# Kernel optimization log

Hardware: AMD Instinct MI355X
Metric: run time of the kernel (lower is better)

## Reference

```python
import jax, jax.numpy as jnp
import numpy as np

N_NODES = 50000
N_PAIRS = 800000
D = 64          # node feature dim
N_BASIS = 8     # basis functions per pair


def setup_inputs() -> dict:
    key = jax.random.key(0)
    k1, k2, k3, k4, k5, k6 = jax.random.split(key, 6)
    p1 = jax.random.normal(k1, (N_NODES, D), dtype=jnp.float32)
    pair_i = jax.random.randint(k2, (N_PAIRS,), 0, N_NODES, dtype=jnp.int64)
    pair_j = jax.random.randint(k3, (N_PAIRS,), 0, N_NODES, dtype=jnp.int64)
    basis = jax.random.normal(k4, (N_PAIRS, N_BASIS), dtype=jnp.float32)
    # bias-free MLP: 64 -> 256 -> 512 (= D * N_BASIS), scaled init
    W1 = jax.random.normal(k5, (D, 256), dtype=jnp.float32) / np.sqrt(D)
    W2 = jax.random.normal(k6, (256, D * N_BASIS), dtype=jnp.float32) / np.sqrt(256.0)
    return {"p1": p1, "pair_i": pair_i, "pair_j": pair_j, "basis": basis,
            "W1": W1, "W2": W2}


def reference(p1, pair_i, pair_j, basis, W1, W2):
    # gather node features for both ends of each pair and sum -> [n_pairs, D]
    inter = p1[pair_i] + p1[pair_j]
    # bias-free FeedForward with tanh between layers
    h = jnp.tanh(inter @ W1)          # [n_pairs, 256]
    h = h @ W2                        # [n_pairs, D * N_BASIS]
    h = h.reshape(-1, p1.shape[-1], basis.shape[-1])  # [n_pairs, D, n_basis]
    out = jnp.einsum('icb,ib->ic', h, basis)          # [n_pairs, D]
    return out[:, None, :]            # [n_pairs, 1, D]
```

## Files before the change

kernel.cpp:

```cpp
#include <hip/hip_runtime.h>

typedef unsigned short u16;
typedef unsigned int   u32;
typedef __bf16 bf16x8 __attribute__((ext_vector_type(8)));
typedef float  f32x4  __attribute__((ext_vector_type(4)));
typedef float  f32x2  __attribute__((ext_vector_type(2)));
typedef unsigned short u16x8 __attribute__((ext_vector_type(8)));
typedef unsigned int   u32x2 __attribute__((ext_vector_type(2)));

#define PPB 128
#define CPB 5

__device__ __forceinline__ u16 f2bf(float f){
  union { float f; u32 i; } v; v.f = f;
  u32 u = v.i;
  u += 0x7fffu + ((u >> 16) & 1u);
  return (u16)(u >> 16);
}
__device__ __forceinline__ float tanh_fast(float x){
  x = fminf(fmaxf(x, -12.f), 12.f);
  float t = __builtin_amdgcn_exp2f(x * 2.885390081777926815f);
  return (t - 1.f) * __builtin_amdgcn_rcpf(t + 1.f);
}

__global__ __launch_bounds__(256) void transpose_cast_k(
    const float* __restrict__ in, u16* __restrict__ out, int R, int C)
{
  __shared__ u16 tile[64][65];
  const int tx = threadIdx.x & 63;
  const int ty = threadIdx.x >> 6;
  const int c0 = blockIdx.x * 64;
  const int r0 = blockIdx.y * 64;
#pragma unroll
  for (int rr = 0; rr < 16; ++rr){
    int r = ty + rr * 4;
    tile[r][tx] = f2bf(in[(size_t)(r0 + r) * C + c0 + tx]);
  }
  __syncthreads();
#pragma unroll
  for (int rr = 0; rr < 16; ++rr){
    int r = ty + rr * 4;
    out[(size_t)(c0 + r) * R + r0 + tx] = tile[tx][r];
  }
}

__global__ __launch_bounds__(256) void w2_block_k(
    const float* __restrict__ in, u16* __restrict__ out)
{
  __shared__ float tile[32][65];
  const int kk = blockIdx.x;
  const int n0 = blockIdx.y * 64;
  const int t  = threadIdx.x;
  {
    int r  = t >> 3;
    int c8 = t & 7;
    const float* src = in + (size_t)(kk*32 + r)*512 + n0 + c8*8;
    f32x4 v0 = *(const f32x4*)src;
    f32x4 v1 = *(const f32x4*)(src + 4);
#pragma unroll
    for (int e = 0; e < 4; ++e){
      tile[r][c8*8 + e]     = v0[e];
      tile[r][c8*8 + 4 + e] = v1[e];
    }
  }
  __syncthreads();
  {
    int c = t >> 2, part = t & 3;
    u16x8 o;
#pragma unroll
    for (int e = 0; e < 8; ++e) o[e] = f2bf(tile[part*8 + e][c]);
    *(u16x8*)(out + ((size_t)kk*512 + n0 + c)*32 + part*8) = o;
  }
}

__global__ __launch_bounds__(1024, 4) void pilayer_kernel(
    const float* __restrict__ p1,
    const int* __restrict__ pair_i,
    const int* __restrict__ pair_j,
    const float* __restrict__ basis,
    const u16* __restrict__ w1t,
    const u16* __restrict__ w2b,
    float* __restrict__ out,
    int n_pairs)
{
  extern __shared__ __align__(16) u16 smem[];
  u16* sh_h  = smem;
  u16* sh_i0 = smem + PPB * 256;
  u16* sh_i1 = sh_i0 + PPB * 64;

  const int tid  = threadIdx.x;
  const int blk  = blockIdx.x;
  const int lane = tid & 63;
  const int w    = tid >> 6;
  const int m16  = lane & 15;
  const int q    = lane >> 4;
  const int sw3  = m16 & 7;
  const int cw   = (w*2 + (q >> 1)) ^ m16;

  bf16x8 awf[8][2];
#pragma unroll
  for (int kk = 0; kk < 8; ++kk)
#pragma unroll
    for (int nt = 0; nt < 2; ++nt)
      awf[kk][nt] = *(const bf16x8*)(
          w2b + ((size_t)kk*512 + w*32 + nt*16 + m16)*32 + q*8);
  const u16* arow = w1t + (size_t)(w*16 + m16)*64 + q*8;
  bf16x8 af0 = *(const bf16x8*)(arow);
  bf16x8 af1 = *(const bf16x8*)(arow + 32);
  __builtin_amdgcn_sched_barrier(0);

  const int pbase = blk * CPB * PPB;
  const int m_g   = tid >> 3;
  const int seg_g = tid & 7;

  {
    int p = pbase + m_g;
    if (p >= n_pairs) p = n_pairs - 1;
    const float* si = p1 + (size_t)pair_i[p]*64 + seg_g*8;
    const float* sj = p1 + (size_t)pair_j[p]*64 + seg_g*8;
    f32x4 a0 = ((const f32x4*)si)[0], a1 = ((const f32x4*)si)[1];
    f32x4 b0 = ((const f32x4*)sj)[0], b1 = ((const f32x4*)sj)[1];
    u16x8 r;
#pragma unroll
    for (int e = 0; e < 4; ++e){
      r[e]     = f2bf(a0[e] + b0[e]);
      r[e + 4] = f2bf(a1[e] + b1[e]);
    }
    *(u16x8*)(sh_i0 + m_g*64 + ((seg_g ^ (m_g & 7)) * 8)) = r;
  }
  __syncthreads();

  u16* sin_cur = sh_i0;
  u16* sin_nxt = sh_i1;
  int nxt_i = 0, nxt_j = 0;

  for (int t = 0; t < CPB; ++t){
    const int pb = pbase + t * PPB;
    const bool pf = (t + 1 < CPB);

    if (pf){
      int pn = pb + PPB + m_g;
      if (pn >= n_pairs) pn = n_pairs - 1;
      nxt_i = pair_i[pn];
      nxt_j = pair_j[pn];
      asm volatile("" : "+v"(nxt_i), "+v"(nxt_j));
    }
    for (int mt1 = 0; mt1 < PPB/16; ++mt1){
      const u16* irow = sin_cur + (size_t)(mt1*16 + m16) * 64;
      bf16x8 b0 = *(const bf16x8*)(irow + ((q ^ sw3) * 8));
      bf16x8 b1 = *(const bf16x8*)(irow + (((q + 4) ^ sw3) * 8));
      f32x4 acc = {0.f, 0.f, 0.f, 0.f};
      acc = __builtin_amdgcn_mfma_f32_16x16x32_bf16(af0, b0, acc, 0, 0, 0);
      acc = __builtin_amdgcn_mfma_f32_16x16x32_bf16(af1, b1, acc, 0, 0, 0);
      u32 lo = (u32)f2bf(tanh_fast(acc[0])) | ((u32)f2bf(tanh_fast(acc[1])) << 16);
      u32 hi = (u32)f2bf(tanh_fast(acc[2])) | ((u32)f2bf(tanh_fast(acc[3])) << 16);
      u32x2 pk = {lo, hi};
      *(u32x2*)(sh_h + (size_t)(mt1*16 + m16)*256 + cw*8 + (q & 1)*4) = pk;
    }
    __syncthreads();

    f32x4 gi0, gi1, gj0, gj1;
    if (pf){
      const float* si = p1 + (size_t)(u32)nxt_i*64 + seg_g*8;
      const float* sj = p1 + (size_t)(u32)nxt_j*64 + seg_g*8;
      gi0 = ((const f32x4*)si)[0]; gi1 = ((const f32x4*)si)[1];
      gj0 = ((const f32x4*)sj)[0]; gj1 = ((const f32x4*)sj)[1];
      asm volatile("" : "+v"(gi0), "+v"(gi1), "+v"(gj0), "+v"(gj1));
    }

    for (int mt = 0; mt < PPB/16; ++mt){
      const int row = mt*16 + m16;
      const int mg  = pb + row;
      const int mgc = (mg < n_pairs) ? mg : (n_pairs - 1);
      f32x4 bb = *(const f32x4*)(basis + (size_t)mgc*8 + (q & 1)*4);

      const u16* hbase = sh_h + (size_t)row * 256;
      f32x4 acc0 = {0.f, 0.f, 0.f, 0.f};
      f32x4 acc1 = {0.f, 0.f, 0.f, 0.f};

      bf16x8 bh = *(const bf16x8*)(hbase + ((q ^ m16) * 8));
#pragma unroll
      for (int kk = 0; kk < 8; ++kk){
        bf16x8 bhn;
        if (kk < 7) bhn = *(const bf16x8*)(hbase + ((((kk + 1)*4 + q) ^ m16) * 8));
        acc0 = __builtin_amdgcn_mfma_f32_16x16x32_bf16(awf[kk][0], bh, acc0, 0, 0, 0);
        acc1 = __builtin_amdgcn_mfma_f32_16x16x32_bf16(awf[kk][1], bh, acc1, 0, 0, 0);
        bh = bhn;
      }

#pragma unroll
      for (int nt = 0; nt < 2; ++nt){
        f32x4 a = (nt == 0) ? acc0 : acc1;
        float s = a[0]*bb[0] + a[1]*bb[1] + a[2]*bb[2] + a[3]*bb[3];
        s += __shfl_xor(s, 16);
        float v2 = __shfl_xor(s, 32);
        if (q == 0 && mg < n_pairs){
          f32x2 pk = {s, v2};
          *(f32x2*)(out + (size_t)mg*64 + w*4 + nt*2) = pk;
        }
      }
    }

    if (pf){
      u16x8 r;
#pragma unroll
      for (int e = 0; e < 4; ++e){
        r[e]     = f2bf(gi0[e] + gj0[e]);
        r[e + 4] = f2bf(gi1[e] + gj1[e]);
      }
      *(u16x8*)(sin_nxt + m_g*64 + ((seg_g ^ (m_g & 7)) * 8)) = r;
    }
    __syncthreads();
    u16* tmp = sin_cur; sin_cur = sin_nxt; sin_nxt = tmp;
  }
}

extern "C" void kernel_launch(void* const* d_in, const int* in_sizes, int n_in,
                              void* d_out, int out_size, void* d_ws, size_t ws_size,
                              hipStream_t stream)
{
  const float* p1    = (const float*)d_in[0];
  const int*   pi    = (const int*)d_in[1];
  const int*   pj    = (const int*)d_in[2];
  const float* basis = (const float*)d_in[3];
  const float* W1    = (const float*)d_in[4];
  const float* W2    = (const float*)d_in[5];
  float* out = (float*)d_out;

  u16* w1t = (u16*)d_ws;
  u16* w2b = w1t + 64 * 256;

  const int n_pairs = in_sizes[1];
  const int lds_bytes = (PPB * 256 + 2 * PPB * 64) * (int)sizeof(u16);

  static int attr_done = 0;
  if (!attr_done){
    hipFuncSetAttribute((const void*)pilayer_kernel,
                        hipFuncAttributeMaxDynamicSharedMemorySize, lds_bytes);
    attr_done = 1;
  }

  transpose_cast_k<<<dim3(4, 1), 256, 0, stream>>>(W1, w1t, 64, 256);
  w2_block_k<<<dim3(8, 8), 256, 0, stream>>>(W2, w2b);

  const int n_chunks = (n_pairs + PPB - 1) / PPB;
  const int blocks   = (n_chunks + CPB - 1) / CPB;
  pilayer_kernel<<<blocks, 1024, lds_bytes, stream>>>(
      p1, pi, pj, basis, w1t, w2b, out, n_pairs);
}
```

Before: 680.0 us.

## Prefetch gathered node rows via direct global-to-LDS loads across chunk pipeline

Replaces the register-staged prefetch of next-chunk node features with global_load_lds async copies into a raw fp32 LDS buffer, issued before the first GEMM. The pair indices are loaded two chunks ahead. Also simplifies tanh (drops the clamp, uses 1-2/(t+1)), switches to hardware bf16 packing, and software-pipelines the basis loads. The goal is to hide gather latency and free VGPRs. The cost is 64KB more LDS per block, which may reduce occupancy, plus an extra barrier per chunk.

```diff
diff --git a/kernel.cpp b/kernel.cpp
--- a/kernel.cpp
+++ b/kernel.cpp
@@ -7,6 +7,7 @@
 typedef float  f32x2  __attribute__((ext_vector_type(2)));
 typedef unsigned short u16x8 __attribute__((ext_vector_type(8)));
 typedef unsigned int   u32x2 __attribute__((ext_vector_type(2)));
+typedef unsigned int   u32x4 __attribute__((ext_vector_type(4)));
 
 #define PPB 128
 #define CPB 5
@@ -17,10 +18,19 @@
   u += 0x7fffu + ((u >> 16) & 1u);
   return (u16)(u >> 16);
 }
+__device__ __forceinline__ u32 pkbf(float lo, float hi){
+  union { __bf16 h[2]; u32 u; } v;
+  v.h[0] = (__bf16)lo; v.h[1] = (__bf16)hi;
+  return v.u;
+}
 __device__ __forceinline__ float tanh_fast(float x){
-  x = fminf(fmaxf(x, -12.f), 12.f);
   float t = __builtin_amdgcn_exp2f(x * 2.885390081777926815f);
-  return (t - 1.f) * __builtin_amdgcn_rcpf(t + 1.f);
+  return __builtin_fmaf(-2.f, __builtin_amdgcn_rcpf(t + 1.f), 1.f);
+}
+__device__ __forceinline__ void gload16(const float* gp, u16* lp){
+  __builtin_amdgcn_global_load_lds(
+      (const __attribute__((address_space(1))) u32*)gp,
+      (__attribute__((address_space(3))) u32*)lp, 16, 0, 0);
 }
 
 __global__ __launch_bounds__(256) void transpose_cast_k(
@@ -84,9 +94,10 @@
     int n_pairs)
 {
   extern __shared__ __align__(16) u16 smem[];
-  u16* sh_h  = smem;
-  u16* sh_i0 = smem + PPB * 256;
-  u16* sh_i1 = sh_i0 + PPB * 64;
+  u16*   sh_h     = smem;
+  u16*   sh_inter = smem + PPB * 256;
+  float* raw      = (float*)(sh_inter + PPB*64);
+  u16*   raw_u16  = (u16*)raw;
 
   const int tid  = threadIdx.x;
   const int blk  = blockIdx.x;
@@ -97,6 +108,13 @@
   const int sw3  = m16 & 7;
   const int cw   = (w*2 + (q >> 1)) ^ m16;
 
+  const int reg_r    = w >> 2;
+  const int reg_half = reg_r & 1;
+  const int* pairsrc = (reg_r >> 1) ? pair_j : pair_i;
+  const int sm0      = (w & 3) * 32;
+  const int sl_m     = lane >> 3;
+  const int sl_c     = lane & 7;
+
   bf16x8 awf[8][2];
 #pragma unroll
   for (int kk = 0; kk < 8; ++kk)
@@ -113,6 +131,17 @@
   const int m_g   = tid >> 3;
   const int seg_g = tid & 7;
 
+  int idxv[4];
+  {
+    int pn = pbase + PPB;
+#pragma unroll
+    for (int i = 0; i < 4; ++i){
+      int m = pn + sm0 + i*8 + sl_m;
+      if (m >= n_pairs) m = n_pairs - 1;
+      idxv[i] = pairsrc[m];
+    }
+  }
+  __builtin_amdgcn_sched_barrier(0);
   {
     int p = pbase + m_g;
     if (p >= n_pairs) p = n_pairs - 1;
@@ -120,98 +149,108 @@
     const float* sj = p1 + (size_t)pair_j[p]*64 + seg_g*8;
     f32x4 a0 = ((const f32x4*)si)[0], a1 = ((const f32x4*)si)[1];
     f32x4 b0 = ((const f32x4*)sj)[0], b1 = ((const f32x4*)sj)[1];
-    u16x8 r;
-#pragma unroll
-    for (int e = 0; e < 4; ++e){
-      r[e]     = f2bf(a0[e] + b0[e]);
-      r[e + 4] = f2bf(a1[e] + b1[e]);
-    }
-    *(u16x8*)(sh_i0 + m_g*64 + ((seg_g ^ (m_g & 7)) * 8)) = r;
+    u32x4 o;
+    o[0] = pkbf(a0[0]+b0[0], a0[1]+b0[1]);
+    o[1] = pkbf(a0[2]+b0[2], a0[3]+b0[3]);
+    o[2] = pkbf(a1[0]+b1[0], a1[1]+b1[1]);
+    o[3] = pkbf(a1[2]+b1[2], a1[3]+b1[3]);
+    *(u32x4*)(sh_inter + m_g*64 + ((seg_g ^ (m_g & 7)) * 8)) = o;
   }
   __syncthreads();
-
-  u16* sin_cur = sh_i0;
-  u16* sin_nxt = sh_i1;
-  int nxt_i = 0, nxt_j = 0;
 
   for (int t = 0; t < CPB; ++t){
     const int pb = pbase + t * PPB;
     const bool pf = (t + 1 < CPB);
 
     if (pf){
-      int pn = pb + PPB + m_g;
-      if (pn >= n_pairs) pn = n_pairs - 1;
-      nxt_i = pair_i[pn];
-      nxt_j = pair_j[pn];
-      asm volatile("" : "+v"(nxt_i), "+v"(nxt_j));
-    }
+#pragma unroll
+      for (int i = 0; i < 4; ++i){
+        const float* gp = p1 + (size_t)(u32)idxv[i]*64 + sl_c*8 + reg_half*4;
+        u16* lp = raw_u16 + reg_r*8192 + (w & 3)*2048 + i*512;
+        gload16(gp, lp);
+      }
+    }
+    __builtin_amdgcn_sched_barrier(0);
+
     for (int mt1 = 0; mt1 < PPB/16; ++mt1){
-      const u16* irow = sin_cur + (size_t)(mt1*16 + m16) * 64;
+      const u16* irow = sh_inter + (size_t)(mt1*16 + m16) * 64;
       bf16x8 b0 = *(const bf16x8*)(irow + ((q ^ sw3) * 8));
       bf16x8 b1 = *(const bf16x8*)(irow + (((q + 4) ^ sw3) * 8));
       f32x4 acc = {0.f, 0.f, 0.f, 0.f};
       acc = __builtin_amdgcn_mfma_f32_16x16x32_bf16(af0, b0, acc, 0, 0, 0);
       acc = __builtin_amdgcn_mfma_f32_16x16x32_bf16(af1, b1, acc, 0, 0, 0);
-      u32 lo = (u32)f2bf(tanh_fast(acc[0])) | ((u32)f2bf(tanh_fast(acc[1])) << 16);
-      u32 hi = (u32)f2bf(tanh_fast(acc[2])) | ((u32)f2bf(tanh_fast(acc[3])) << 16);
-      u32x2 pk = {lo, hi};
+      u32x2 pk;
+      pk[0] = pkbf(tanh_fast(acc[0]), tanh_fast(acc[1]));
+      pk[1] = pkbf(tanh_fast(acc[2]), tanh_fast(acc[3]));
       *(u32x2*)(sh_h + (size_t)(mt1*16 + m16)*256 + cw*8 + (q & 1)*4) = pk;
     }
     __syncthreads();
 
-    f32x4 gi0, gi1, gj0, gj1;
+    {
+      int mg0c = pb + m16; if (mg0c >= n_pairs) mg0c = n_pairs - 1;
+      f32x4 bb = *(const f32x4*)(basis + (size_t)mg0c*8 + (q & 1)*4);
+      for (int mt = 0; mt < PPB/16; ++mt){
+        const int row = mt*16 + m16;
+        const int mg  = pb + row;
+        f32x4 bbn;
+        if (mt < 7){
+          int mgn = mg + 16; if (mgn >= n_pairs) mgn = n_pairs - 1;
+          bbn = *(const f32x4*)(basis + (size_t)mgn*8 + (q & 1)*4);
+        }
+
+        const u16* hbase = sh_h + (size_t)row * 256;
+        f32x4 acc0 = {0.f, 0.f, 0.f, 0.f};
+        f32x4 acc1 = {0.f, 0.f, 0.f, 0.f};
+
+        bf16x8 bh = *(const bf16x8*)(hbase + ((q ^ m16) * 8));
+#pragma unroll
+        for (int kk = 0; kk < 8; ++kk){
+          bf16x8 bhn;
+          if (kk < 7) bhn = *(const bf16x8*)(hbase + ((((kk + 1)*4 + q) ^ m16) * 8));
+          acc0 = __builtin_amdgcn_mfma_f32_16x16x32_bf16(awf[kk][0], bh, acc0, 0, 0, 0);
+          acc1 = __builtin_amdgcn_mfma_f32_16x16x32_bf16(awf[kk][1], bh, acc1, 0, 0, 0);
+          bh = bhn;
+        }
+
+#pragma unroll
+        for (int nt = 0; nt < 2; ++nt){
+          f32x4 a = (nt == 0) ? acc0 : acc1;
+          float s = a[0]*bb[0] + a[1]*bb[1] + a[2]*bb[2] + a[3]*bb[3];
+          s += __shfl_xor(s, 16);
+          float v2 = __shfl_xor(s, 32);
+          if (q == 0 && mg < n_pairs){
+            f32x2 pk = {s, v2};
+            *(f32x2*)(out + (size_t)mg*64 + w*4 + nt*2) = pk;
+          }
+        }
+        bb = bbn;
+      }
+    }
+    __syncthreads();
+
     if (pf){
-      const float* si = p1 + (size_t)(u32)nxt_i*64 + seg_g*8;
-      const float* sj = p1 + (size_t)(u32)nxt_j*64 + seg_g*8;
-      gi0 = ((const f32x4*)si)[0]; gi1 = ((const f32x4*)si)[1];
-      gj0 = ((const f32x4*)sj)[0]; gj1 = ((const f32x4*)sj)[1];
-      asm volatile("" : "+v"(gi0), "+v"(gi1), "+v"(gj0), "+v"(gj1));
-    }
-
-    for (int mt = 0; mt < PPB/16; ++mt){
-      const int row = mt*16 + m16;
-      const int mg  = pb + row;
-      const int mgc = (mg < n_pairs) ? mg : (n_pairs - 1);
-      f32x4 bb = *(const f32x4*)(basis + (size_t)mgc*8 + (q & 1)*4);
-
-      const u16* hbase = sh_h + (size_t)row * 256;
-      f32x4 acc0 = {0.f, 0.f, 0.f, 0.f};
-      f32x4 acc1 = {0.f, 0.f, 0.f, 0.f};
-
-      bf16x8 bh = *(const bf16x8*)(hbase + ((q ^ m16) * 8));
-#pragma unroll
-      for (int kk = 0; kk < 8; ++kk){
-        bf16x8 bhn;
-        if (kk < 7) bhn = *(const bf16x8*)(hbase + ((((kk + 1)*4 + q) ^ m16) * 8));
-        acc0 = __builtin_amdgcn_mfma_f32_16x16x32_bf16(awf[kk][0], bh, acc0, 0, 0, 0);
-        acc1 = __builtin_amdgcn_mfma_f32_16x16x32_bf16(awf[kk][1], bh, acc1, 0, 0, 0);
-        bh = bhn;
+      if (t + 2 < CPB){
+        int pn2 = pb + 2*PPB;
+#pragma unroll
+        for (int i = 0; i < 4; ++i){
+          int m = pn2 + sm0 + i*8 + sl_m;
+          if (m >= n_pairs) m = n_pairs - 1;
+          idxv[i] = pairsrc[m];
+        }
       }
-
-#pragma unroll
-      for (int nt = 0; nt < 2; ++nt){
-        f32x4 a = (nt == 0) ? acc0 : acc1;
-        float s = a[0]*bb[0] + a[1]*bb[1] + a[2]*bb[2] + a[3]*bb[3];
-        s += __shfl_xor(s, 16);
-        float v2 = __shfl_xor(s, 32);
-        if (q == 0 && mg < n_pairs){
-          f32x2 pk = {s, v2};
-          *(f32x2*)(out + (size_t)mg*64 + w*4 + nt*2) = pk;
-        }
-      }
-    }
-
-    if (pf){
-      u16x8 r;
-#pragma unroll
-      for (int e = 0; e < 4; ++e){
-        r[e]     = f2bf(gi0[e] + gj0[e]);
-        r[e + 4] = f2bf(gi1[e] + gj1[e]);
-      }
-      *(u16x8*)(sin_nxt + m_g*64 + ((seg_g ^ (m_g & 7)) * 8)) = r;
-    }
-    __syncthreads();
-    u16* tmp = sin_cur; sin_cur = sin_nxt; sin_nxt = tmp;
+      __builtin_amdgcn_sched_barrier(0);
+      f32x4 iA = *(const f32x4*)(raw +         tid*4);
+      f32x4 iB = *(const f32x4*)(raw +  4096 + tid*4);
+      f32x4 jA = *(const f32x4*)(raw +  8192 + tid*4);
+      f32x4 jB = *(const f32x4*)(raw + 12288 + tid*4);
+      u32x4 o;
+      o[0] = pkbf(iA[0]+jA[0], iA[1]+jA[1]);
+      o[1] = pkbf(iA[2]+jA[2], iA[3]+jA[3]);
+      o[2] = pkbf(iB[0]+jB[0], iB[1]+jB[1]);
+      o[3] = pkbf(iB[2]+jB[2], iB[3]+jB[3]);
+      *(u32x4*)(sh_inter + m_g*64 + ((seg_g ^ (m_g & 7)) * 8)) = o;
+      __syncthreads();
+    }
   }
 }
 
@@ -231,7 +270,7 @@
   u16* w2b = w1t + 64 * 256;
 
   const int n_pairs = in_sizes[1];
-  const int lds_bytes = (PPB * 256 + 2 * PPB * 64) * (int)sizeof(u16);
+  const int lds_bytes = PPB*256*2 + PPB*64*2 + 65536;
 
   static int attr_done = 0;
   if (!attr_done){
```

Result: slower. 1.039 ms (+52.8%).

## Switch MLP to fp16 MFMA and pre-convert node features to fp16 in workspace

Applied to the files above, without the earlier changes.

Moves the weights, activations and MFMA instructions from bf16 to fp16, and replaces the bf16 rounding helper with native fp16 conversion and packing. When the workspace is large enough, a new pre-pass converts p1 to fp16, which halves the bytes fetched by the random per-pair gathers. The tanh is simplified to a single fma-plus-reciprocal form and its clamp is dropped. In exchange this adds an extra pass over p1 and fp16 range risks, and the unclamped tanh could produce NaN for large negative inputs.

```diff
diff --git a/kernel.cpp b/kernel.cpp
--- a/kernel.cpp
+++ b/kernel.cpp
@@ -2,28 +2,43 @@
 
 typedef unsigned short u16;
 typedef unsigned int   u32;
-typedef __bf16 bf16x8 __attribute__((ext_vector_type(8)));
+typedef _Float16 f16x8 __attribute__((ext_vector_type(8)));
 typedef float  f32x4  __attribute__((ext_vector_type(4)));
 typedef float  f32x2  __attribute__((ext_vector_type(2)));
 typedef unsigned short u16x8 __attribute__((ext_vector_type(8)));
 typedef unsigned int   u32x2 __attribute__((ext_vector_type(2)));
+typedef unsigned int   u32x4 __attribute__((ext_vector_type(4)));
 
 #define PPB 128
 #define CPB 5
 
-__device__ __forceinline__ u16 f2bf(float f){
-  union { float f; u32 i; } v; v.f = f;
-  u32 u = v.i;
-  u += 0x7fffu + ((u >> 16) & 1u);
-  return (u16)(u >> 16);
+__device__ __forceinline__ u32 pkf16(float lo, float hi){
+  union { _Float16 h[2]; u32 u; } v;
+  v.h[0] = (_Float16)lo; v.h[1] = (_Float16)hi;
+  return v.u;
 }
 __device__ __forceinline__ float tanh_fast(float x){
-  x = fminf(fmaxf(x, -12.f), 12.f);
   float t = __builtin_amdgcn_exp2f(x * 2.885390081777926815f);
-  return (t - 1.f) * __builtin_amdgcn_rcpf(t + 1.f);
-}
-
-__global__ __launch_bounds__(256) void transpose_cast_k(
+  return __builtin_fmaf(-2.f, __builtin_amdgcn_rcpf(t + 1.f), 1.f);
+}
+
+__global__ __launch_bounds__(256) void p1_to_f16_k(
+    const float* __restrict__ in, u16* __restrict__ out, int n8)
+{
+  int t = blockIdx.x * 256 + threadIdx.x;
+  if (t >= n8) return;
+  f32x4 v0 = *(const f32x4*)(in + (size_t)t*8);
+  f32x4 v1 = *(const f32x4*)(in + (size_t)t*8 + 4);
+  u16x8 o;
+  union { _Float16 h; u16 u; } c;
+#pragma unroll
+  for (int e = 0; e < 4; ++e){ c.h = (_Float16)v0[e]; o[e]   = c.u; }
+#pragma unroll
+  for (int e = 0; e < 4; ++e){ c.h = (_Float16)v1[e]; o[e+4] = c.u; }
+  *(u16x8*)(out + (size_t)t*8) = o;
+}
+
+__global__ __launch_bounds__(256) void transpose_cast_f16_k(
     const float* __restrict__ in, u16* __restrict__ out, int R, int C)
 {
   __shared__ u16 tile[64][65];
@@ -31,10 +46,12 @@
   const int ty = threadIdx.x >> 6;
   const int c0 = blockIdx.x * 64;
   const int r0 = blockIdx.y * 64;
+  union { _Float16 h; u16 u; } c;
 #pragma unroll
   for (int rr = 0; rr < 16; ++rr){
     int r = ty + rr * 4;
-    tile[r][tx] = f2bf(in[(size_t)(r0 + r) * C + c0 + tx]);
+    c.h = (_Float16)in[(size_t)(r0 + r) * C + c0 + tx];
+    tile[r][tx] = c.u;
   }
   __syncthreads();
 #pragma unroll
@@ -44,7 +61,7 @@
   }
 }
 
-__global__ __launch_bounds__(256) void w2_block_k(
+__global__ __launch_bounds__(256) void w2_block_f16_k(
     const float* __restrict__ in, u16* __restrict__ out)
 {
   __shared__ float tile[32][65];
@@ -67,14 +84,34 @@
   {
     int c = t >> 2, part = t & 3;
     u16x8 o;
-#pragma unroll
-    for (int e = 0; e < 8; ++e) o[e] = f2bf(tile[part*8 + e][c]);
+    union { _Float16 h; u16 u; } cc;
+#pragma unroll
+    for (int e = 0; e < 8; ++e){ cc.h = (_Float16)tile[part*8 + e][c]; o[e] = cc.u; }
     *(u16x8*)(out + ((size_t)kk*512 + n0 + c)*32 + part*8) = o;
   }
 }
 
+template<bool USE_H>
+__device__ __forceinline__ f16x8 ld_p1row(const float* p1, const u16* p1h,
+                                          u32 idx, int seg){
+  if constexpr (USE_H){
+    union { u16x8 u; f16x8 h; } v;
+    v.u = *(const u16x8*)(p1h + (size_t)idx*64 + seg*8);
+    return v.h;
+  } else {
+    const f32x4* s = (const f32x4*)(p1 + (size_t)idx*64 + seg*8);
+    f32x4 a = s[0], b = s[1];
+    f16x8 r;
+#pragma unroll
+    for (int e = 0; e < 4; ++e){ r[e] = (_Float16)a[e]; r[e+4] = (_Float16)b[e]; }
+    return r;
+  }
+}
+
+template<bool USE_H>
 __global__ __launch_bounds__(1024, 4) void pilayer_kernel(
     const float* __restrict__ p1,
+    const u16* __restrict__ p1h,
     const int* __restrict__ pair_i,
     const int* __restrict__ pair_j,
     const float* __restrict__ basis,
@@ -97,16 +134,16 @@
   const int sw3  = m16 & 7;
   const int cw   = (w*2 + (q >> 1)) ^ m16;
 
-  bf16x8 awf[8][2];
+  f16x8 awf[8][2];
 #pragma unroll
   for (int kk = 0; kk < 8; ++kk)
 #pragma unroll
     for (int nt = 0; nt < 2; ++nt)
-      awf[kk][nt] = *(const bf16x8*)(
+      awf[kk][nt] = *(const f16x8*)(
           w2b + ((size_t)kk*512 + w*32 + nt*16 + m16)*32 + q*8);
   const u16* arow = w1t + (size_t)(w*16 + m16)*64 + q*8;
-  bf16x8 af0 = *(const bf16x8*)(arow);
-  bf16x8 af1 = *(const bf16x8*)(arow + 32);
+  f16x8 af0 = *(const f16x8*)(arow);
+  f16x8 af1 = *(const f16x8*)(arow + 32);
   __builtin_amdgcn_sched_barrier(0);
 
   const int pbase = blk * CPB * PPB;
@@ -116,57 +153,49 @@
   {
     int p = pbase + m_g;
     if (p >= n_pairs) p = n_pairs - 1;
-    const float* si = p1 + (size_t)pair_i[p]*64 + seg_g*8;
-    const float* sj = p1 + (size_t)pair_j[p]*64 + seg_g*8;
-    f32x4 a0 = ((const f32x4*)si)[0], a1 = ((const f32x4*)si)[1];
-    f32x4 b0 = ((const f32x4*)sj)[0], b1 = ((const f32x4*)sj)[1];
-    u16x8 r;
-#pragma unroll
-    for (int e = 0; e < 4; ++e){
-      r[e]     = f2bf(a0[e] + b0[e]);
-      r[e + 4] = f2bf(a1[e] + b1[e]);
-    }
-    *(u16x8*)(sh_i0 + m_g*64 + ((seg_g ^ (m_g & 7)) * 8)) = r;
+    f16x8 vi = ld_p1row<USE_H>(p1, p1h, (u32)pair_i[p], seg_g);
+    f16x8 vj = ld_p1row<USE_H>(p1, p1h, (u32)pair_j[p], seg_g);
+    union { f16x8 h; u32x4 u; } sv; sv.h = vi + vj;
+    *(u32x4*)(sh_i0 + m_g*64 + ((seg_g ^ (m_g & 7)) * 8)) = sv.u;
   }
   __syncthreads();
 
   u16* sin_cur = sh_i0;
   u16* sin_nxt = sh_i1;
-  int nxt_i = 0, nxt_j = 0;
 
   for (int t = 0; t < CPB; ++t){
     const int pb = pbase + t * PPB;
     const bool pf = (t + 1 < CPB);
 
+    int nxt_i = 0, nxt_j = 0;
     if (pf){
       int pn = pb + PPB + m_g;
       if (pn >= n_pairs) pn = n_pairs - 1;
       nxt_i = pair_i[pn];
       nxt_j = pair_j[pn];
-      asm volatile("" : "+v"(nxt_i), "+v"(nxt_j));
-    }
+    }
+    __builtin_amdgcn_sched_barrier(0);
+
     for (int mt1 = 0; mt1 < PPB/16; ++mt1){
       const u16* irow = sin_cur + (size_t)(mt1*16 + m16) * 64;
-      bf16x8 b0 = *(const bf16x8*)(irow + ((q ^ sw3) * 8));
-      bf16x8 b1 = *(const bf16x8*)(irow + (((q + 4) ^ sw3) * 8));
+      f16x8 b0 = *(const f16x8*)(irow + ((q ^ sw3) * 8));
+      f16x8 b1 = *(const f16x8*)(irow + (((q + 4) ^ sw3) * 8));
       f32x4 acc = {0.f, 0.f, 0.f, 0.f};
-      acc = __builtin_amdgcn_mfma_f32_16x16x32_bf16(af0, b0, acc, 0, 0, 0);
-      acc = __builtin_amdgcn_mfma_f32_16x16x32_bf16(af1, b1, acc, 0, 0, 0);
-      u32 lo = (u32)f2bf(tanh_fast(acc[0])) | ((u32)f2bf(tanh_fast(acc[1])) << 16);
-      u32 hi = (u32)f2bf(tanh_fast(acc[2])) | ((u32)f2bf(tanh_fast(acc[3])) << 16);
-      u32x2 pk = {lo, hi};
+      acc = __builtin_amdgcn_mfma_f32_16x16x32_f16(af0, b0, acc, 0, 0, 0);
+      acc = __builtin_amdgcn_mfma_f32_16x16x32_f16(af1, b1, acc, 0, 0, 0);
+      u32x2 pk;
+      pk[0] = pkf16(tanh_fast(acc[0]), tanh_fast(acc[1]));
+      pk[1] = pkf16(tanh_fast(acc[2]), tanh_fast(acc[3]));
       *(u32x2*)(sh_h + (size_t)(mt1*16 + m16)*256 + cw*8 + (q & 1)*4) = pk;
     }
     __syncthreads();
 
-    f32x4 gi0, gi1, gj0, gj1;
+    f16x8 vi, vj;
     if (pf){
-      const float* si = p1 + (size_t)(u32)nxt_i*64 + seg_g*8;
-      const float* sj = p1 + (size_t)(u32)nxt_j*64 + seg_g*8;
-      gi0 = ((const f32x4*)si)[0]; gi1 = ((const f32x4*)si)[1];
-      gj0 = ((const f32x4*)sj)[0]; gj1 = ((const f32x4*)sj)[1];
-      asm volatile("" : "+v"(gi0), "+v"(gi1), "+v"(gj0), "+v"(gj1));
-    }
+      vi = ld_p1row<USE_H>(p1, p1h, (u32)nxt_i, seg_g);
+      vj = ld_p1row<USE_H>(p1, p1h, (u32)nxt_j, seg_g);
+    }
+    __builtin_amdgcn_sched_barrier(0);
 
     for (int mt = 0; mt < PPB/16; ++mt){
       const int row = mt*16 + m16;
@@ -178,13 +207,13 @@
       f32x4 acc0 = {0.f, 0.f, 0.f, 0.f};
       f32x4 acc1 = {0.f, 0.f, 0.f, 0.f};
 
-      bf16x8 bh = *(const bf16x8*)(hbase + ((q ^ m16) * 8));
+      f16x8 bh = *(const f16x8*)(hbase + ((q ^ m16) * 8));
 #pragma unroll
       for (int kk = 0; kk < 8; ++kk){
-        bf16x8 bhn;
-        if (kk < 7) bhn = *(const bf16x8*)(hbase + ((((kk + 1)*4 + q) ^ m16) * 8));
-        acc0 = __builtin_amdgcn_mfma_f32_16x16x32_bf16(awf[kk][0], bh, acc0, 0, 0, 0);
-        acc1 = __builtin_amdgcn_mfma_f32_16x16x32_bf16(awf[kk][1], bh, acc1, 0, 0, 0);
+        f16x8 bhn;
+        if (kk < 7) bhn = *(const f16x8*)(hbase + ((((kk + 1)*4 + q) ^ m16) * 8));
+        acc0 = __builtin_amdgcn_mfma_f32_16x16x32_f16(awf[kk][0], bh, acc0, 0, 0, 0);
+        acc1 = __builtin_amdgcn_mfma_f32_16x16x32_f16(awf[kk][1], bh, acc1, 0, 0, 0);
         bh = bhn;
       }
 
@@ -202,13 +231,8 @@
     }
 
     if (pf){
-      u16x8 r;
-#pragma unroll
-      for (int e = 0; e < 4; ++e){
-        r[e]     = f2bf(gi0[e] + gj0[e]);
-        r[e + 4] = f2bf(gi1[e] + gj1[e]);
-      }
-      *(u16x8*)(sin_nxt + m_g*64 + ((seg_g ^ (m_g & 7)) * 8)) = r;
+      union { f16x8 h; u32x4 u; } sv; sv.h = vi + vj;
+      *(u32x4*)(sin_nxt + m_g*64 + ((seg_g ^ (m_g & 7)) * 8)) = sv.u;
     }
     __syncthreads();
     u16* tmp = sin_cur; sin_cur = sin_nxt; sin_nxt = tmp;
@@ -227,24 +251,39 @@
   const float* W2    = (const float*)d_in[5];
   float* out = (float*)d_out;
 
+  const int n_pairs = in_sizes[1];
+  const int n_nodes = in_sizes[0] / 64;
+
   u16* w1t = (u16*)d_ws;
   u16* w2b = w1t + 64 * 256;
-
-  const int n_pairs = in_sizes[1];
+  u16* p1h = w2b + 8 * 512 * 32;
+  const size_t need = (size_t)(64*256 + 8*512*32 + (size_t)n_nodes*64) * sizeof(u16);
+  const bool use_h = (ws_size >= need);
+
   const int lds_bytes = (PPB * 256 + 2 * PPB * 64) * (int)sizeof(u16);
 
   static int attr_done = 0;
   if (!attr_done){
-    hipFuncSetAttribute((const void*)pilayer_kernel,
+    hipFuncSetAttribute((const void*)pilayer_kernel<true>,
+                        hipFuncAttributeMaxDynamicSharedMemorySize, lds_bytes);
+    hipFuncSetAttribute((const void*)pilayer_kernel<false>,
                         hipFuncAttributeMaxDynamicSharedMemorySize, lds_bytes);
     attr_done = 1;
   }
 
-  transpose_cast_k<<<dim3(4, 1), 256, 0, stream>>>(W1, w1t, 64, 256);
-  w2_block_k<<<dim3(8, 8), 256, 0, stream>>>(W2, w2b);
+  transpose_cast_f16_k<<<dim3(4, 1), 256, 0, stream>>>(W1, w1t, 64, 256);
+  w2_block_f16_k<<<dim3(8, 8), 256, 0, stream>>>(W2, w2b);
+  if (use_h){
+    const int n8 = n_nodes * 8;
+    p1_to_f16_k<<<(n8 + 255)/256, 256, 0, stream>>>(p1, p1h, n8);
+  }
 
   const int n_chunks = (n_pairs + PPB - 1) / PPB;
   const int blocks   = (n_chunks + CPB - 1) / CPB;
-  pilayer_kernel<<<blocks, 1024, lds_bytes, stream>>>(
-      p1, pi, pj, basis, w1t, w2b, out, n_pairs);
-}
+  if (use_h)
+    pilayer_kernel<true><<<blocks, 1024, lds_bytes, stream>>>(
+        p1, p1h, pi, pj, basis, w1t, w2b, out, n_pairs);
+  else
+    pilayer_kernel<false><<<blocks, 1024, lds_bytes, stream>>>(
+        p1, nullptr, pi, pj, basis, w1t, w2b, out, n_pairs);
+}
```

Result: slower. 833.3 us (+22.6%).
